# Optimization experiments

Hardware: AMD Instinct MI355X
Metric: run time of the kernel (lower is better)

The kernel has to match this reference:

```python
import jax, jax.numpy as jnp
import numpy as np

N_NODES = 100000
N_EDGES = 3200000
IN_CH = 128
HID = 32


def setup_inputs() -> dict:
    key = jax.random.key(0)
    k1, k2, k3, k4 = jax.random.split(key, 4)
    x = jax.random.normal(k1, (N_NODES, IN_CH), dtype=jnp.float32)
    edge_index = jax.random.randint(k2, (2, N_EDGES), 0, N_NODES, dtype=jnp.int64)
    # Glorot-style scale for weights
    W1 = jax.random.normal(k3, (IN_CH, HID), dtype=jnp.float32) * (1.0 / np.sqrt(IN_CH))
    b1 = jnp.zeros((HID,), dtype=jnp.float32)
    W2 = jax.random.normal(k4, (HID, HID), dtype=jnp.float32) * (1.0 / np.sqrt(HID))
    b2 = jnp.zeros((HID,), dtype=jnp.float32)
    return {"x": x, "edge_index": edge_index, "W1": W1, "b1": b1, "W2": W2, "b2": b2}


def _gcn_conv(x, src, dst, norm, W, b, n_nodes):
    # PyG GCNConv: h = x @ W, then symmetric-normalized scatter-add, then + bias
    h = x @ W                                   # [N, out]
    msg = h[src] * norm[:, None]                # gather + per-edge scale
    out = jax.ops.segment_sum(msg, dst, num_segments=n_nodes)  # scatter-add
    return out + b


def reference(x, edge_index, W1, b1, W2, b2):
    n = x.shape[0]
    loop = jnp.arange(n, dtype=edge_index.dtype)
    # add self-loops (PyG default add_self_loops=True)
    src = jnp.concatenate([edge_index[0], loop])
    dst = jnp.concatenate([edge_index[1], loop])
    # symmetric normalization deg^-1/2 on destination-side in-degree (incl. self-loops)
    deg = jax.ops.segment_sum(jnp.ones_like(dst, dtype=x.dtype), dst, num_segments=n)
    dinv = jnp.where(deg > 0, jax.lax.rsqrt(deg), 0.0)
    norm = dinv[src] * dinv[dst]                # [E + N]
    h = _gcn_conv(x, src, dst, norm, W1, b1, n)
    h = jax.nn.relu(h)
    out = _gcn_conv(h, src, dst, norm, W2, b2, n)
    return out
```

## Files before the change

### kernel.cpp

```cpp
#include <hip/hip_runtime.h>
#include <hip/hip_bf16.h>

#define N_NODES 100000
#define N_EDGES 3200000
#define IN_CH   128
#define HID     32
#define NB      1024
#define NPB     98
#define CAP     4096
#define CHUNK   4096
#define EPT     8
#define ACC_LD  33
#define NPASS   8
#define OCTN    12500u
#define FXS     1048576.0f
#define FXI     (1.0f/1048576.0f)
#define NTILE   6250
#define TPW     2

__device__ __forceinline__ unsigned int pack_bf16x2(float a, float b) {
    unsigned int ua = __float_as_uint(a);
    unsigned int ub = __float_as_uint(b);
    ua = (ua + 0x7FFFu + ((ua >> 16) & 1u)) >> 16;
    ub = (ub + 0x7FFFu + ((ub >> 16) & 1u)) >> 16;
    return (ua & 0xFFFFu) | (ub << 16);
}
__device__ __forceinline__ float bf_lo(unsigned int v) { return __uint_as_float(v << 16); }
__device__ __forceinline__ float bf_hi(unsigned int v) { return __uint_as_float(v & 0xFFFF0000u); }
__device__ __forceinline__ int   f2fx(float f)         { return (int)(f * FXS); }
__device__ __forceinline__ float hif(float f) {
    return __uint_as_float(__float_as_uint(f) & 0xFFFF0000u);
}
__device__ __forceinline__ unsigned int tpack(float a, float b) {
    return (__float_as_uint(a) >> 16) | (__float_as_uint(b) & 0xFFFF0000u);
}
__device__ __forceinline__ unsigned short bf16_rne(float f) {
    unsigned int u = __float_as_uint(f);
    return (unsigned short)((u + 0x7FFFu + ((u >> 16) & 1u)) >> 16);
}

typedef short bf16x8 __attribute__((ext_vector_type(8)));
typedef float f32x4  __attribute__((ext_vector_type(4)));
union frag_u { bf16x8 f; unsigned int u[4]; };

__global__ __launch_bounds__(256) void detect_idx(const int* __restrict__ ei,
                                                  int* __restrict__ flag) {
    __shared__ int nz;
    if (threadIdx.x == 0) nz = 0;
    __syncthreads();
    if (ei[2 * threadIdx.x + 1] != 0) atomicAdd(&nz, 1);
    __syncthreads();
    if (threadIdx.x == 0) flag[0] = (nz == 0) ? 1 : 0;
}

__device__ __forceinline__ int edge_at(const int* __restrict__ ei, int idx64,
                                       size_t pos) {
    if (idx64) return (int)((const long long*)ei)[pos];
    return ei[pos];
}

__global__ __launch_bounds__(256) void bcur_init(int* __restrict__ bcur) {
    int b = blockIdx.x * 256 + threadIdx.x;
    if (b < NB) bcur[b] = b * CAP;
}

__global__ __launch_bounds__(512) void bucket_scatter5(
    const int* __restrict__ ei,
    const int* __restrict__ flag,
    int* __restrict__ bcur,
    unsigned int* __restrict__ ebuf) {
    __shared__ int cnt[NB];
    __shared__ int loff[NB];
    __shared__ int dlt[NB];
    __shared__ int tmp[512];
    __shared__ unsigned int   sbuf[CHUNK];
    __shared__ unsigned short sbb[CHUNK];

    int t = threadIdx.x;
    for (int j = t; j < NB; j += 512) cnt[j] = 0;
    __syncthreads();

    int e0 = blockIdx.x * CHUNK;
    int nE = N_EDGES - e0; if (nE > CHUNK) nE = CHUNK;
    int idx64 = flag[0];

    unsigned int rs[EPT], rd[EPT];
#pragma unroll
    for (int j = 0; j < EPT; ++j) {
        int i = t + j * 512;
        if (i < nE) {
            rs[j] = (unsigned int)edge_at(ei, idx64, (size_t)(e0 + i));
            rd[j] = (unsigned int)edge_at(ei, idx64, (size_t)N_EDGES + e0 + i);
        }
    }

#pragma unroll
    for (int j = 0; j < EPT; ++j) {
        int i = t + j * 512;
        if (i < nE) atomicAdd(&cnt[rd[j] / NPB], 1);
    }
    __syncthreads();

    int c0 = cnt[2 * t], c1 = cnt[2 * t + 1];
    int s = c0 + c1;
    tmp[t] = s;
    __syncthreads();
    for (int off = 1; off < 512; off <<= 1) {
        int x = 0;
        if (t >= off) x = tmp[t - off];
        __syncthreads();
        if (t >= off) tmp[t] += x;
        __syncthreads();
    }
    int base = tmp[t] - s;
    loff[2 * t]     = base;
    loff[2 * t + 1] = base + c0;
    __syncthreads();

    for (int j = t; j < NB; j += 512) {
        int c = cnt[j];
        int gb = (c > 0) ? atomicAdd(&bcur[j], c) : 0;
        dlt[j] = gb - loff[j];
        cnt[j] = 0;
    }
    __syncthreads();

#pragma unroll
    for (int j = 0; j < EPT; ++j) {
        int i = t + j * 512;
        if (i < nE) {
            unsigned int b = rd[j] / NPB;
            int pos = loff[b] + atomicAdd(&cnt[b], 1);
            sbuf[pos] = (rs[j] << 8) | (rd[j] - b * NPB);
            sbb[pos]  = (unsigned short)b;
        }
    }
    __syncthreads();

    for (int i = t; i < nE; i += 512)
        ebuf[dlt[sbb[i]] + i] = sbuf[i];
}

__global__ __launch_bounds__(512) void finalize_csr(
    const int* __restrict__ bcur,
    unsigned int* __restrict__ ebuf,
    float* __restrict__ dinv,
    int* __restrict__ octp) {
    __shared__ unsigned int lbuf[CAP];
    __shared__ unsigned int sbuf[CAP];
    __shared__ int lhist[NPB];
    __shared__ int oh[8];
    __shared__ int obase[9];
    __shared__ int ocur[8];
    int b = blockIdx.x, t = threadIdx.x;
    int n0 = b * NPB;
    int nn = N_NODES - n0; if (nn > NPB) nn = NPB; if (nn < 0) nn = 0;
    int cnt = bcur[b] - b * CAP;
    unsigned int* reg = ebuf + (size_t)b * CAP;

    for (int j = t; j < NPB; j += 512) lhist[j] = 0;
    if (t < 8) oh[t] = 0;
    __syncthreads();

    for (int i = t; i < cnt; i += 512) {
        unsigned int e = reg[i];
        lbuf[i] = e;
        atomicAdd(&lhist[e & 255u], 1);
        atomicAdd(&oh[(e >> 8) / OCTN], 1);
    }
    __syncthreads();

    for (int j = t; j < nn; j += 512)
        dinv[n0 + j] = rsqrtf((float)(lhist[j] + 1));

    if (t == 0) {
        obase[0] = 0;
        for (int p = 0; p < 8; ++p) {
            obase[p + 1] = obase[p] + oh[p];
            ocur[p] = obase[p];
        }
    }
    __syncthreads();

    for (int i = t; i < cnt; i += 512) {
        unsigned int e = lbuf[i];
        int p = (int)((e >> 8) / OCTN);
        int pos = atomicAdd(&ocur[p], 1);
        sbuf[pos] = e;
    }
    __syncthreads();

    for (int i = t; i < cnt; i += 512)
        reg[i] = sbuf[i];
    if (t < 9) octp[b * 9 + t] = obase[t];
}

__global__ __launch_bounds__(256) void gemm1_mfma(
    const float* __restrict__ x,
    const float* __restrict__ W1,
    const float* __restrict__ dinv,
    unsigned short* __restrict__ h1u) {
    int wv   = blockIdx.x * 4 + (threadIdx.x >> 6);
    int lane = threadIdx.x & 63;
    int lq   = lane & 15;
    int kh   = lane >> 4;

    frag_u bh[2][4], bl[2][4];
#pragma unroll
    for (int t = 0; t < 2; ++t) {
#pragma unroll
        for (int s = 0; s < 4; ++s) {
            int ch = t * 16 + lq;
            int k0 = s * 32 + kh * 8;
            float w[8], wh[8];
#pragma unroll
            for (int i = 0; i < 8; ++i) {
                w[i]  = W1[(k0 + i) * HID + ch];
                wh[i] = hif(w[i]);
            }
#pragma unroll
            for (int j = 0; j < 4; ++j) {
                bh[t][s].u[j] = tpack(wh[2 * j], wh[2 * j + 1]);
                bl[t][s].u[j] = tpack(w[2 * j] - wh[2 * j],
                                      w[2 * j + 1] - wh[2 * j + 1]);
            }
        }
    }

#pragma unroll 1
    for (int it = 0; it < TPW; ++it) {
        int tile = wv * TPW + it;
        if (tile >= NTILE) return;
        int n0 = tile * 16;
        const float* xr = x + (size_t)(n0 + lq) * IN_CH;

        f32x4 acc0 = {0.f, 0.f, 0.f, 0.f};
        f32x4 acc1 = {0.f, 0.f, 0.f, 0.f};
#pragma unroll
        for (int s = 0; s < 4; ++s) {
            int k0 = s * 32 + kh * 8;
            float4 v0 = *reinterpret_cast<const float4*>(xr + k0);
            float4 v1 = *reinterpret_cast<const float4*>(xr + k0 + 4);
            frag_u ah, al;
            ah.u[0] = tpack(v0.x, v0.y);
            ah.u[1] = tpack(v0.z, v0.w);
            ah.u[2] = tpack(v1.x, v1.y);
            ah.u[3] = tpack(v1.z, v1.w);
            al.u[0] = tpack(v0.x - hif(v0.x), v0.y - hif(v0.y));
            al.u[1] = tpack(v0.z - hif(v0.z), v0.w - hif(v0.w));
            al.u[2] = tpack(v1.x - hif(v1.x), v1.y - hif(v1.y));
            al.u[3] = tpack(v1.z - hif(v1.z), v1.w - hif(v1.w));

            acc0 = __builtin_amdgcn_mfma_f32_16x16x32_bf16(ah.f, bh[0][s].f, acc0, 0, 0, 0);
            acc0 = __builtin_amdgcn_mfma_f32_16x16x32_bf16(al.f, bh[0][s].f, acc0, 0, 0, 0);
            acc0 = __builtin_amdgcn_mfma_f32_16x16x32_bf16(ah.f, bl[0][s].f, acc0, 0, 0, 0);
            acc1 = __builtin_amdgcn_mfma_f32_16x16x32_bf16(ah.f, bh[1][s].f, acc1, 0, 0, 0);
            acc1 = __builtin_amdgcn_mfma_f32_16x16x32_bf16(al.f, bh[1][s].f, acc1, 0, 0, 0);
            acc1 = __builtin_amdgcn_mfma_f32_16x16x32_bf16(ah.f, bl[1][s].f, acc1, 0, 0, 0);
        }

#pragma unroll
        for (int j = 0; j < 4; ++j) {
            int node = n0 + kh * 4 + j;
            float dn = dinv[node];
            unsigned short* dst = h1u + (size_t)node * 32 + lq;
            dst[0]  = bf16_rne(acc0[j] * dn);
            dst[16] = bf16_rne(acc1[j] * dn);
        }
    }
}

__device__ __forceinline__ uint4 row_q(const unsigned int* __restrict__ hb,
                                       unsigned int s, int q4) {
    return *reinterpret_cast<const uint4*>(hb + (size_t)s * 16 + q4);
}

__device__ __forceinline__ void fx_scatter8(int* acc, unsigned int e,
                                            int co, uint4 v) {
    int* a = acc + (int)(e & 255u) * ACC_LD + co;
    atomicAdd(&a[0], f2fx(bf_lo(v.x))); atomicAdd(&a[1], f2fx(bf_hi(v.x)));
    atomicAdd(&a[2], f2fx(bf_lo(v.y))); atomicAdd(&a[3], f2fx(bf_hi(v.y)));
    atomicAdd(&a[4], f2fx(bf_lo(v.z))); atomicAdd(&a[5], f2fx(bf_hi(v.z)));
    atomicAdd(&a[6], f2fx(bf_lo(v.w))); atomicAdd(&a[7], f2fx(bf_hi(v.w)));
}

__global__ __launch_bounds__(512, 8) void agg1_srt(
    const int* __restrict__ bcur,
    const unsigned int* __restrict__ ebuf,
    const int* __restrict__ octp,
    const unsigned int* __restrict__ h1b,
    const float* __restrict__ dinv,
    const float* __restrict__ b1,
    const float* __restrict__ W2,
    unsigned int* __restrict__ h3b) {
    __shared__ int acc[NPB * ACC_LD];
    __shared__ float w2s[HID * HID];
    __shared__ float b1s[HID];
    int b = blockIdx.x, t = threadIdx.x;
    int n0 = b * NPB;
    int nn = N_NODES - n0; if (nn > NPB) nn = NPB; if (nn < 0) nn = 0;
    const unsigned int* reg = ebuf + (size_t)b * CAP;

    for (int i = t; i < HID * HID; i += 512) w2s[i] = W2[i];
    if (t < HID) b1s[t] = b1[t];

    for (int u = t; u < nn * 4; u += 512) {
        int n = u >> 2, q = u & 3;
        uint4 sv = *reinterpret_cast<const uint4*>(h1b + (size_t)(n0 + n) * 16 + 4 * q);
        int* a = &acc[n * ACC_LD + 8 * q];
        a[0] = f2fx(bf_lo(sv.x)); a[1] = f2fx(bf_hi(sv.x));
        a[2] = f2fx(bf_lo(sv.y)); a[3] = f2fx(bf_hi(sv.y));
        a[4] = f2fx(bf_lo(sv.z)); a[5] = f2fx(bf_hi(sv.z));
        a[6] = f2fx(bf_lo(sv.w)); a[7] = f2fx(bf_hi(sv.w));
    }
    __syncthreads();

    int q4 = (t & 3) * 4;
    int co = (t & 3) * 8;
#pragma unroll 1
    for (int p = 0; p < NPASS; ++p) {
        int o1 = octp[b * 9 + p + 1];
        int i  = octp[b * 9 + p] + (t >> 2);
        for (; i + 128 < o1; i += 256) {
            unsigned int e0 = reg[i];
            unsigned int e1 = reg[i + 128];
            uint4 v0 = row_q(h1b, e0 >> 8, q4);
            uint4 v1 = row_q(h1b, e1 >> 8, q4);
            fx_scatter8(acc, e0, co, v0);
            fx_scatter8(acc, e1, co, v1);
        }
        if (i < o1) {
            unsigned int e = reg[i];
            uint4 v = row_q(h1b, e >> 8, q4);
            fx_scatter8(acc, e, co, v);
        }
    }
    __syncthreads();

    float* h2s = (float*)acc;
    for (int u = t; u < nn * HID; u += 512) {
        int n = u >> 5, j = u & 31;
        float v = (float)acc[n * ACC_LD + j] * FXI * dinv[n0 + n] + b1s[j];
        h2s[n * ACC_LD + j] = v > 0.f ? v : 0.f;
    }
    __syncthreads();

    for (int u = t; u < nn * 4; u += 512) {
        int n = u >> 2, qq = u & 3;
        const float* h2 = &h2s[n * ACC_LD];
        float a2[8];
#pragma unroll
        for (int k = 0; k < 8; ++k) a2[k] = 0.f;
#pragma unroll
        for (int j = 0; j < HID; ++j) {
            float hj = h2[j];
            const float* wr = &w2s[j * HID + 8 * qq];
#pragma unroll
            for (int k = 0; k < 8; ++k) a2[k] += hj * wr[k];
        }
        float dn = dinv[n0 + n];
        unsigned int* dst = h3b + (size_t)(n0 + n) * 16 + 4 * qq;
        *reinterpret_cast<uint4*>(dst) = make_uint4(
            pack_bf16x2(a2[0] * dn, a2[1] * dn),
            pack_bf16x2(a2[2] * dn, a2[3] * dn),
            pack_bf16x2(a2[4] * dn, a2[5] * dn),
            pack_bf16x2(a2[6] * dn, a2[7] * dn));
    }
}

__global__ __launch_bounds__(512, 8) void agg2_srt(
    const int* __restrict__ bcur,
    const unsigned int* __restrict__ ebuf,
    const int* __restrict__ octp,
    const unsigned int* __restrict__ h3b,
    const float* __restrict__ dinv,
    const float* __restrict__ b2,
    float* __restrict__ out) {
    __shared__ int acc[NPB * ACC_LD];
    __shared__ float b2s[HID];
    int b = blockIdx.x, t = threadIdx.x;
    int n0 = b * NPB;
    int nn = N_NODES - n0; if (nn > NPB) nn = NPB; if (nn < 0) nn = 0;
    const unsigned int* reg = ebuf + (size_t)b * CAP;

    if (t < HID) b2s[t] = b2[t];

    for (int u = t; u < nn * 4; u += 512) {
        int n = u >> 2, q = u & 3;
        uint4 sv = *reinterpret_cast<const uint4*>(h3b + (size_t)(n0 + n) * 16 + 4 * q);
        int* a = &acc[n * ACC_LD + 8 * q];
        a[0] = f2fx(bf_lo(sv.x)); a[1] = f2fx(bf_hi(sv.x));
        a[2] = f2fx(bf_lo(sv.y)); a[3] = f2fx(bf_hi(sv.y));
        a[4] = f2fx(bf_lo(sv.z)); a[5] = f2fx(bf_hi(sv.z));
        a[6] = f2fx(bf_lo(sv.w)); a[7] = f2fx(bf_hi(sv.w));
    }
    __syncthreads();

    int q4 = (t & 3) * 4;
    int co = (t & 3) * 8;
#pragma unroll 1
    for (int p = 0; p < NPASS; ++p) {
        int o1 = octp[b * 9 + p + 1];
        int i  = octp[b * 9 + p] + (t >> 2);
        for (; i + 128 < o1; i += 256) {
            unsigned int e0 = reg[i];
            unsigned int e1 = reg[i + 128];
            uint4 v0 = row_q(h3b, e0 >> 8, q4);
            uint4 v1 = row_q(h3b, e1 >> 8, q4);
            fx_scatter8(acc, e0, co, v0);
            fx_scatter8(acc, e1, co, v1);
        }
        if (i < o1) {
            unsigned int e = reg[i];
            uint4 v = row_q(h3b, e >> 8, q4);
            fx_scatter8(acc, e, co, v);
        }
    }
    __syncthreads();

    for (int u = t; u < nn * 4; u += 512) {
        int n = u >> 2, qq = u & 3;
        float dn = dinv[n0 + n];
        const int* a = &acc[n * ACC_LD + 8 * qq];
        const float* bb = &b2s[8 * qq];
        float4 o1v, o2v;
        o1v.x = (float)a[0] * FXI * dn + bb[0];
        o1v.y = (float)a[1] * FXI * dn + bb[1];
        o1v.z = (float)a[2] * FXI * dn + bb[2];
        o1v.w = (float)a[3] * FXI * dn + bb[3];
        o2v.x = (float)a[4] * FXI * dn + bb[4];
        o2v.y = (float)a[5] * FXI * dn + bb[5];
        o2v.z = (float)a[6] * FXI * dn + bb[6];
        o2v.w = (float)a[7] * FXI * dn + bb[7];
        float* op = out + (size_t)(n0 + n) * 32 + 8 * qq;
        *reinterpret_cast<float4*>(op)     = o1v;
        *reinterpret_cast<float4*>(op + 4) = o2v;
    }
}

extern "C" void kernel_launch(void* const* d_in, const int* in_sizes, int n_in,
                              void* d_out, int out_size, void* d_ws, size_t ws_size,
                              hipStream_t stream) {
    const float* x  = (const float*)d_in[0];
    const int*   ei = (const int*)d_in[1];
    const float* W1 = (const float*)d_in[2];
    const float* b1 = (const float*)d_in[3];
    const float* W2 = (const float*)d_in[4];
    const float* b2 = (const float*)d_in[5];
    float* out = (float*)d_out;

    int*          flag = (int*)d_ws;
    int*          bcur = flag + 64;
    int*          octp = bcur + NB;
    float*        dinv = (float*)(octp + NB * 9);
    unsigned int* ebuf = (unsigned int*)(dinv + N_NODES);
    unsigned int* h1b  = ebuf + (size_t)NB * CAP;
    unsigned int* h3b  = h1b + (size_t)N_NODES * 16;

    const int chunkBlocks = (N_EDGES + CHUNK - 1) / CHUNK;
    const int g1Blocks    = (NTILE + 4 * TPW - 1) / (4 * TPW);

    detect_idx<<<1, 256, 0, stream>>>(ei, flag);

    bcur_init<<<(NB + 255) / 256, 256, 0, stream>>>(bcur);
    bucket_scatter5<<<chunkBlocks, 512, 0, stream>>>(ei, flag, bcur, ebuf);
    finalize_csr<<<NB, 512, 0, stream>>>(bcur, ebuf, dinv, octp);

    gemm1_mfma<<<g1Blocks, 256, 0, stream>>>(x, W1, dinv,
                                             (unsigned short*)h1b);
    agg1_srt<<<NB, 512, 0, stream>>>(bcur, ebuf, octp, h1b, dinv, b1, W2, h3b);

    agg2_srt<<<NB, 512, 0, stream>>>(bcur, ebuf, octp, h3b, dinv, b2, out);
}
```

Before: 218.3 us.

## Replace global atomic bucket offsets with histogram-matrix and per-bucket scan

Bucket offsets were claimed with global atomicAdd on bcur during the scatter. They are now computed deterministically: a histogram kernel writes per-chunk bucket counts into a matrix, a scan kernel prefix-sums each bucket column, and the scatter reads precomputed offsets. This removes contended global atomics and makes edge order stable, at the cost of an extra pass over dst indices and two more launches. finalize_csr also drops to 256 threads per block.

```diff
diff --git a/kernel.cpp b/kernel.cpp
--- a/kernel.cpp
+++ b/kernel.cpp
@@ -9,6 +9,7 @@
 #define NPB     98
 #define CAP     4096
 #define CHUNK   4096
+#define NBLK    ((N_EDGES + CHUNK - 1) / CHUNK)
 #define EPT     8
 #define ACC_LD  33
 #define NPASS   8
@@ -59,15 +60,65 @@
     return ei[pos];
 }
 
-__global__ __launch_bounds__(256) void bcur_init(int* __restrict__ bcur) {
-    int b = blockIdx.x * 256 + threadIdx.x;
-    if (b < NB) bcur[b] = b * CAP;
-}
-
-__global__ __launch_bounds__(512) void bucket_scatter5(
+__global__ __launch_bounds__(256) void hist_k(
     const int* __restrict__ ei,
     const int* __restrict__ flag,
-    int* __restrict__ bcur,
+    int* __restrict__ hmat) {
+    __shared__ int cnt[NB];
+    int t = threadIdx.x;
+    for (int j = t; j < NB; j += 256) cnt[j] = 0;
+    __syncthreads();
+
+    int e0 = blockIdx.x * CHUNK;
+    int nE = N_EDGES - e0; if (nE > CHUNK) nE = CHUNK;
+    int idx64 = flag[0];
+
+    for (int i = t; i < nE; i += 256) {
+        unsigned int d = (unsigned int)edge_at(ei, idx64, (size_t)N_EDGES + e0 + i);
+        atomicAdd(&cnt[d / NPB], 1);
+    }
+    __syncthreads();
+
+    int* row = hmat + (size_t)blockIdx.x * NB;
+    for (int j = t; j < NB; j += 256) row[j] = cnt[j];
+}
+
+__global__ __launch_bounds__(256) void scan_k(
+    const int* __restrict__ hmat,
+    int* __restrict__ gofs,
+    int* __restrict__ bcur) {
+    __shared__ int tsum[256];
+    int b = blockIdx.x, t = threadIdx.x;
+
+    int v[4]; int s = 0;
+#pragma unroll
+    for (int j = 0; j < 4; ++j) {
+        int i = t * 4 + j;
+        v[j] = (i < NBLK) ? hmat[(size_t)i * NB + b] : 0;
+        s += v[j];
+    }
+    tsum[t] = s;
+    __syncthreads();
+    for (int off = 1; off < 256; off <<= 1) {
+        int x = 0;
+        if (t >= off) x = tsum[t - off];
+        __syncthreads();
+        if (t >= off) tsum[t] += x;
+        __syncthreads();
+    }
+    int run = tsum[t] - s + b * CAP;
+#pragma unroll
+    for (int j = 0; j < 4; ++j) {
+        int i = t * 4 + j;
+        if (i < NBLK) { gofs[(size_t)i * NB + b] = run; run += v[j]; }
+    }
+    if (t == 255) bcur[b] = run;
+}
+
+__global__ __launch_bounds__(512) void scatter6(
+    const int* __restrict__ ei,
+    const int* __restrict__ flag,
+    const int* __restrict__ gofs,
     unsigned int* __restrict__ ebuf) {
     __shared__ int cnt[NB];
     __shared__ int loff[NB];
@@ -117,10 +168,9 @@
     loff[2 * t + 1] = base + c0;
     __syncthreads();
 
+    const int* grow = gofs + (size_t)blockIdx.x * NB;
     for (int j = t; j < NB; j += 512) {
-        int c = cnt[j];
-        int gb = (c > 0) ? atomicAdd(&bcur[j], c) : 0;
-        dlt[j] = gb - loff[j];
+        dlt[j] = grow[j] - loff[j];
         cnt[j] = 0;
     }
     __syncthreads();
@@ -141,7 +191,7 @@
         ebuf[dlt[sbb[i]] + i] = sbuf[i];
 }
 
-__global__ __launch_bounds__(512) void finalize_csr(
+__global__ __launch_bounds__(256) void finalize_csr(
     const int* __restrict__ bcur,
     unsigned int* __restrict__ ebuf,
     float* __restrict__ dinv,
@@ -158,11 +208,11 @@
     int cnt = bcur[b] - b * CAP;
     unsigned int* reg = ebuf + (size_t)b * CAP;
 
-    for (int j = t; j < NPB; j += 512) lhist[j] = 0;
+    for (int j = t; j < NPB; j += 256) lhist[j] = 0;
     if (t < 8) oh[t] = 0;
     __syncthreads();
 
-    for (int i = t; i < cnt; i += 512) {
+    for (int i = t; i < cnt; i += 256) {
         unsigned int e = reg[i];
         lbuf[i] = e;
         atomicAdd(&lhist[e & 255u], 1);
@@ -170,7 +220,7 @@
     }
     __syncthreads();
 
-    for (int j = t; j < nn; j += 512)
+    for (int j = t; j < nn; j += 256)
         dinv[n0 + j] = rsqrtf((float)(lhist[j] + 1));
 
     if (t == 0) {
@@ -182,7 +232,7 @@
     }
     __syncthreads();
 
-    for (int i = t; i < cnt; i += 512) {
+    for (int i = t; i < cnt; i += 256) {
         unsigned int e = lbuf[i];
         int p = (int)((e >> 8) / OCTN);
         int pos = atomicAdd(&ocur[p], 1);
@@ -190,7 +240,7 @@
     }
     __syncthreads();
 
-    for (int i = t; i < cnt; i += 512)
+    for (int i = t; i < cnt; i += 256)
         reg[i] = sbuf[i];
     if (t < 9) octp[b * 9 + t] = obase[t];
 }
@@ -456,15 +506,17 @@
     unsigned int* ebuf = (unsigned int*)(dinv + N_NODES);
     unsigned int* h1b  = ebuf + (size_t)NB * CAP;
     unsigned int* h3b  = h1b + (size_t)N_NODES * 16;
-
-    const int chunkBlocks = (N_EDGES + CHUNK - 1) / CHUNK;
-    const int g1Blocks    = (NTILE + 4 * TPW - 1) / (4 * TPW);
+    int*          hmat = (int*)h1b;
+    int*          gofs = (int*)h3b;
+
+    const int g1Blocks = (NTILE + 4 * TPW - 1) / (4 * TPW);
 
     detect_idx<<<1, 256, 0, stream>>>(ei, flag);
 
-    bcur_init<<<(NB + 255) / 256, 256, 0, stream>>>(bcur);
-    bucket_scatter5<<<chunkBlocks, 512, 0, stream>>>(ei, flag, bcur, ebuf);
-    finalize_csr<<<NB, 512, 0, stream>>>(bcur, ebuf, dinv, octp);
+    hist_k<<<NBLK, 256, 0, stream>>>(ei, flag, hmat);
+    scan_k<<<NB, 256, 0, stream>>>(hmat, gofs, bcur);
+    scatter6<<<NBLK, 512, 0, stream>>>(ei, flag, gofs, ebuf);
+    finalize_csr<<<NB, 256, 0, stream>>>(bcur, ebuf, dinv, octp);
 
     gemm1_mfma<<<g1Blocks, 256, 0, stream>>>(x, W1, dinv,
                                              (unsigned short*)h1b);
```

Measured after the change: 223.4 us. 1.02x slower.
